# Kernel tuning notes

Measured on AMD Instinct MI355X. Metric: run time of the kernel, lower is better.

The kernel has to match this reference:

```python
import jax, jax.numpy as jnp
import numpy as np

# Sizes from init_kwargs / input_specs
D_MODEL = 1024; D_INT = 64; KW = 32; B = 2; L = 4096
SAMPLING = np.array([5, 5, 2, 1, 1]); DILATIONS = np.array([1, 1, 2, 4, 8])
SUBHEADS = len(SAMPLING); HEADS = int(SAMPLING.sum())  # 5, 14
HEAD_OF_SUB = np.repeat(np.arange(SUBHEADS), SAMPLING)  # subhead index for each head
HEAD_DIL = np.repeat(DILATIONS, SAMPLING)                # dilation for each head


def _win_idx(dil):
    # centered dilated band, clipped at sequence edges -> [L, KW]
    offs = (np.arange(KW) - KW // 2) * dil
    return np.clip(np.arange(L)[:, None] + offs[None, :], 0, L - 1)

SUB_IDX = jnp.asarray(np.stack([_win_idx(d) for d in DILATIONS]))  # [SUBHEADS, L, KW]
HEAD_IDX = jnp.asarray(np.stack([_win_idx(d) for d in HEAD_DIL]))  # [HEADS, L, KW]


def setup_inputs() -> dict:
    rng = jax.random.key(0)
    ks = jax.random.split(rng, 9)
    n = lambda i, sh, sc=1.0: jax.random.normal(ks[i], sh, dtype=jnp.float32) * sc
    return dict(
        query=n(0, (B, L, D_MODEL)),
        key=n(1, (B, L, D_MODEL)),
        value=n(2, (B, L, D_MODEL)),
        Wq=n(3, (SUBHEADS, D_MODEL, D_INT), 0.02),
        bq=jnp.zeros((SUBHEADS, D_INT), jnp.float32),
        Wk=n(4, (SUBHEADS, D_MODEL, D_INT), 0.02),
        bk=jnp.zeros((SUBHEADS, D_INT), jnp.float32),
        Wv=n(5, (HEADS, D_MODEL, D_INT), 0.02),
        bv=jnp.zeros((HEADS, D_INT), jnp.float32),
        Ws=n(6, (HEADS, KW, KW), 0.05) + jnp.eye(KW, dtype=jnp.float32)[None],
        bs=jnp.zeros((HEADS, KW), jnp.float32),
        Wc=n(7, (HEADS * D_INT, D_MODEL), 0.02),
        bc=jnp.zeros((D_MODEL,), jnp.float32),
    )


def reference(query, key, value, Wq, bq, Wk, bk, Wv, bv, Ws, bs, Wc, bc):
    # per-subhead query/key projections: [S, B, L, Di]
    q = jnp.einsum('bld,sdi->sbli', query, Wq) + bq[:, None, None, :]
    k = jnp.einsum('bld,sdi->sbli', key, Wk) + bk[:, None, None, :]
    # per-head value projection: [H, B, L, Di]
    v = jnp.einsum('bld,hdi->hbli', value, Wv) + bv[:, None, None, :]
    # dilated banded key windows per subhead: [S, B, L, KW, Di]
    kw = jax.vmap(lambda kh, ix: kh[:, ix], in_axes=(0, 0))(k, SUB_IDX)
    # banded scores [S, B, L, KW]
    scores = jnp.einsum('sbli,sblki->sblk', q, kw) / jnp.sqrt(jnp.float32(D_INT))
    # supersample: replicate each subhead's scores to its heads -> [H, B, L, KW]
    scores_h = scores[HEAD_OF_SUB]
    # per-head positional supersampling linear on the score window
    sampled = jnp.einsum('hblk,hkm->hblm', scores_h, Ws) + bs[:, None, None, :]
    attn = jax.nn.softmax(sampled, axis=-1)
    # dilated value windows per head: [H, B, L, KW, Di]
    vw = jax.vmap(lambda vh, ix: vh[:, ix], in_axes=(0, 0))(v, HEAD_IDX)
    out = jnp.einsum('hblk,hblki->hbli', attn, vw)  # [H, B, L, Di]
    out = jnp.transpose(out, (1, 2, 0, 3)).reshape(B, L, HEADS * D_INT)
    return out @ Wc + bc  # [B, L, D_MODEL]
```

## Files before the change

kernel.cpp:

```cpp
#include <hip/hip_runtime.h>
#include <math.h>

#define D_MODEL 1024
#define D_INT   64
#define KW      32
#define L_SEQ   4096
#define SUBHEADS 5
#define HEADS   14
#define M_ROWS  8192
#define N_CAT   896
#define NQK     320

typedef unsigned short us;
typedef unsigned int   uu;
typedef __attribute__((ext_vector_type(4))) unsigned int uu4;
typedef __attribute__((ext_vector_type(8))) short bf16x8_t;
typedef __attribute__((ext_vector_type(4))) float f32x4_t;

__device__ __forceinline__ float u2f(uu u) {
    float f; __builtin_memcpy(&f, &u, 4); return f;
}
__device__ __forceinline__ float blo(uu u) { return u2f(u << 16); }
__device__ __forceinline__ float bhi(uu u) { return u2f(u & 0xffff0000u); }
__device__ __forceinline__ us f2b(float f) {
    uu u; __builtin_memcpy(&u, &f, 4);
    u += 0x7fffu + ((u >> 16) & 1u);
    return (us)(u >> 16);
}
__device__ __forceinline__ uu pack2(float a, float b) {
    return (uu)f2b(a) | ((uu)f2b(b) << 16);
}
__device__ __forceinline__ uu cvtpk(float a, float b) {
    uu r;
    asm("v_cvt_pk_bf16_f32 %0, %1, %2" : "=v"(r) : "v"(a), "v"(b));
    return r;
}
__device__ __forceinline__ void load16(void* lds, const void* g) {
    __builtin_amdgcn_global_load_lds(
        (const __attribute__((address_space(1))) unsigned int*)g,
        (__attribute__((address_space(3))) unsigned int*)lds, 16, 0, 0);
}
__device__ __forceinline__ int subhead_of(int h) {
    return (h < 5) ? 0 : (h < 10) ? 1 : (h < 12) ? 2 : (h == 12) ? 3 : 4;
}
__device__ __forceinline__ int dil_of_sub(int s) {
    return (s <= 1) ? 1 : (1 << (s - 1));
}

#define CAST_BLK 1536
__global__ __launch_bounds__(256)
void prep_kernel(const float4* __restrict__ q, const float4* __restrict__ k,
                 const float4* __restrict__ v,
                 const float* __restrict__ Wq, const float* __restrict__ Wk,
                 const float* __restrict__ Wv, const float* __restrict__ Wc,
                 us* __restrict__ Xq, us* __restrict__ Xk, us* __restrict__ Xv,
                 us* __restrict__ Wqt, us* __restrict__ Wkt,
                 us* __restrict__ Wvt, us* __restrict__ Wct)
{
    __shared__ float t[32][33];
    const int tid = threadIdx.x;
    const int b = blockIdx.x;

    if (b < CAST_BLK) {
        const int arr = b >> 9;
        const int blk = b & 511;
        const float4* s = (arr == 0) ? q : (arr == 1) ? k : v;
        uu4* d = (uu4*)((arr == 0) ? Xq : (arr == 1) ? Xk : Xv);
        const int tg = blk * 256 + tid;
#pragma unroll
        for (int it = 0; it < 8; it++) {
            const int i = tg + it * 131072;
            float4 x0 = s[2 * i];
            float4 x1 = s[2 * i + 1];
            uu4 o;
            o.x = cvtpk(x0.x, x0.y); o.y = cvtpk(x0.z, x0.w);
            o.z = cvtpk(x1.x, x1.y); o.w = cvtpk(x1.z, x1.w);
            d[i] = o;
        }
        return;
    }

    int g = b - CAST_BLK;
    const float* S; us* D; int K, N;
    if (g < 640) {
        if (g < 320) { S = Wq; D = Wqt; } else { S = Wk; D = Wkt; g -= 320; }
        K = 1024; N = 64;
    } else if (g < 1536) {
        g -= 640; S = Wv; D = Wvt; K = 1024; N = 64;
    } else {
        g -= 1536; S = Wc; D = Wct; K = 896; N = 1024;
    }
    const int nkx = K >> 5;
    const int kx = g % nkx;
    const int rest = g / nkx;
    const int ny = rest % (N >> 5);
    const int z  = rest / (N >> 5);
    const int k0 = kx * 32, n0 = ny * 32;
    S += (size_t)z * K * N;
    D += (size_t)z * K * N;
    const int tx = tid & 31, ty = tid >> 5;
#pragma unroll
    for (int r = 0; r < 32; r += 8)
        t[r + ty][tx] = S[(size_t)(k0 + r + ty) * N + n0 + tx];
    __syncthreads();
#pragma unroll
    for (int r = 0; r < 32; r += 8)
        D[(size_t)(n0 + r + ty) * K + k0 + tx] = f2b(t[tx][r + ty]);
}

__device__ __forceinline__
void gemm64_core(const us* __restrict__ A, const us* __restrict__ Bt,
                 const float* __restrict__ bias, us* __restrict__ C,
                 int K, int ldC, int row0, int col0, us* As, us* Bs)
{
    const int tid = threadIdx.x, w = tid >> 6, lane = tid & 63;
    const int m = lane & 15, quad = lane >> 4;
    const int sr = lane >> 3;
    const int scs = (lane & 7) ^ sr;

    f32x4_t z4 = {0.f, 0.f, 0.f, 0.f};
    f32x4_t acc[2][4] = {{z4, z4, z4, z4}, {z4, z4, z4, z4}};

    for (int k0 = 0; k0 < K; k0 += 64) {
#pragma unroll
        for (int p = 0; p < 4; p++) {
            const int r = w * 32 + p * 8 + sr;
            load16(&As[(w * 32 + p * 8) * 64], A + (size_t)(row0 + r) * K + k0 + scs * 8);
        }
#pragma unroll
        for (int p = 0; p < 2; p++) {
            const int r = w * 16 + p * 8 + sr;
            load16(&Bs[(w * 16 + p * 8) * 64], Bt + (size_t)(col0 + r) * K + k0 + scs * 8);
        }
        __syncthreads();
#pragma unroll
        for (int ks = 0; ks < 2; ks++) {
            const int slot = ((ks * 4 + quad) ^ (m & 7)) * 8;
            bf16x8_t a0 = *(const bf16x8_t*)&As[(w * 32 + m) * 64 + slot];
            bf16x8_t a1 = *(const bf16x8_t*)&As[(w * 32 + 16 + m) * 64 + slot];
#pragma unroll
            for (int t = 0; t < 4; t++) {
                bf16x8_t bb = *(const bf16x8_t*)&Bs[(t * 16 + m) * 64 + slot];
                acc[0][t] = __builtin_amdgcn_mfma_f32_16x16x32_bf16(a0, bb, acc[0][t], 0, 0, 0);
                acc[1][t] = __builtin_amdgcn_mfma_f32_16x16x32_bf16(a1, bb, acc[1][t], 0, 0, 0);
            }
        }
        __syncthreads();
    }

#pragma unroll
    for (int tm = 0; tm < 2; tm++) {
        const int rbase = row0 + w * 32 + tm * 16 + quad * 4;
#pragma unroll
        for (int t = 0; t < 4; t++) {
            const int col = col0 + t * 16 + m;
            const float bi = bias[col];
#pragma unroll
            for (int r = 0; r < 4; r++)
                C[(size_t)(rbase + r) * ldC + col] = f2b(acc[tm][t][r] + bi);
        }
    }
}

__device__ __forceinline__
void gemm128_core(const us* __restrict__ A, const us* __restrict__ Bt,
                  const float* __restrict__ bias, void* __restrict__ Cv,
                  int K, int ldC, int outBf16, int row0, int col0,
                  us* As, us* Bs)
{
    const int tid = threadIdx.x, w = tid >> 6, lane = tid & 63;
    const int m = lane & 15, quad = lane >> 4;
    const int sr = lane >> 3;
    const int scs = (lane & 7) ^ sr;
    const int mrow0 = (w & 1) * 64, ncol0 = (w >> 1) * 64;

    f32x4_t z = {0.f, 0.f, 0.f, 0.f};
    f32x4_t acc[4][4] = {{z,z,z,z},{z,z,z,z},{z,z,z,z},{z,z,z,z}};

    for (int k0 = 0; k0 < K; k0 += 64) {
#pragma unroll
        for (int p = 0; p < 4; p++) {
            const int r = w * 32 + p * 8 + sr;
            load16(&As[(w * 32 + p * 8) * 64], A  + (size_t)(row0 + r) * K + k0 + scs * 8);
            load16(&Bs[(w * 32 + p * 8) * 64], Bt + (size_t)(col0 + r) * K + k0 + scs * 8);
        }
        __syncthreads();
#pragma unroll
        for (int ks = 0; ks < 2; ks++) {
            const int slot = ((ks * 4 + quad) ^ (m & 7)) * 8;
            bf16x8_t a[4], b[4];
#pragma unroll
            for (int t = 0; t < 4; t++) {
                a[t] = *(const bf16x8_t*)&As[(mrow0 + t * 16 + m) * 64 + slot];
                b[t] = *(const bf16x8_t*)&Bs[(ncol0 + t * 16 + m) * 64 + slot];
            }
#pragma unroll
            for (int i = 0; i < 4; i++)
#pragma unroll
                for (int j = 0; j < 4; j++)
                    acc[i][j] = __builtin_amdgcn_mfma_f32_16x16x32_bf16(a[i], b[j], acc[i][j], 0, 0, 0);
        }
        __syncthreads();
    }

#pragma unroll
    for (int i = 0; i < 4; i++) {
        const int rbase = row0 + mrow0 + i * 16 + quad * 4;
        if (outBf16) {
            us* Cb = (us*)Cv;
#pragma unroll
            for (int j = 0; j < 4; j++) {
                const int col = col0 + ncol0 + j * 16 + m;
                const float bi = bias[col];
#pragma unroll
                for (int r = 0; r < 4; r++)
                    Cb[(size_t)(rbase + r) * ldC + col] = f2b(acc[i][j][r] + bi);
            }
        } else {
            float* Cb = (float*)Cv;
#pragma unroll
            for (int j = 0; j < 4; j++) {
                const int col = col0 + ncol0 + j * 16 + m;
                const float bi = bias[col];
#pragma unroll
                for (int r = 0; r < 4; r++)
                    Cb[(size_t)(rbase + r) * ldC + col] = acc[i][j][r] + bi;
            }
        }
    }
}

__global__ __launch_bounds__(256)
void proj_kernel(const us* __restrict__ Xq, const us* __restrict__ Xk,
                 const us* __restrict__ Xv,
                 const us* __restrict__ Wqt, const us* __restrict__ Wkt,
                 const us* __restrict__ Wvt,
                 const float* __restrict__ bq, const float* __restrict__ bk,
                 const float* __restrict__ bv,
                 us* __restrict__ qbuf, us* __restrict__ kbuf,
                 us* __restrict__ vbuf)
{
    __shared__ us As[128 * 64];
    __shared__ us Bs[128 * 64];
    const int b = blockIdx.x;
    if (b < 448) {
        const int bx = b & 63, cy = b >> 6;
        gemm128_core(Xv, Wvt, bv, vbuf, D_MODEL, N_CAT, 1,
                     bx << 7, cy << 7, As, Bs);
    } else {
        const int idx = b - 448;
        const int bx = idx & 63;
        const int rest = idx >> 6;
        const int cy = rest % 5, z = rest / 5;
        gemm64_core(z ? Xk : Xq, z ? Wkt : Wqt, z ? bk : bq,
                    z ? kbuf : qbuf, D_MODEL, NQK,
                    bx << 7, cy << 6, As, Bs);
    }
}

__global__ __launch_bounds__(256)
void gemm_out(const us* __restrict__ ab, const us* __restrict__ Wct,
              const float* __restrict__ bc, float* __restrict__ out)
{
    __shared__ us As[128 * 64];
    __shared__ us Bs[128 * 64];
    gemm128_core(ab, Wct, bc, out, N_CAT, D_MODEL, 0,
                 (int)(blockIdx.x << 7), (int)(blockIdx.y << 7), As, Bs);
}

template<int ROWS>
__global__ __launch_bounds__(256)
void score_kernel(const us* __restrict__ qb, const us* __restrict__ kb,
                  float* __restrict__ scores, int sbase)
{
    __shared__ uu kslab[ROWS * 36];
    __shared__ uu qslab[64 * 32];

    const int tid  = threadIdx.x;
    const int wave = tid >> 6;
    const int lane = tid & 63;
    const int j    = lane & 31;
    const int half = lane >> 5;
    const int s    = sbase + blockIdx.y;
    const int d    = dil_of_sub(s);
    const int ml0  = blockIdx.x * 64;
    const int l0   = ml0 & 4095;
    const int bm   = ml0 - l0;
    const int W    = 64 + 31 * d;

    const uu* kg = (const uu*)kb;
    const uu* qg = (const uu*)qb;

    for (int idx = tid; idx < W * 32; idx += 256) {
        int r = idx >> 5, c = idx & 31;
        int src = l0 - 16 * d + r;
        src = src < 0 ? 0 : (src > 4095 ? 4095 : src);
        kslab[r * 36 + c] = kg[(size_t)(bm + src) * 160 + s * 32 + c];
    }
    for (int idx = tid; idx < 64 * 32; idx += 256) {
        int r = idx >> 5, c = idx & 31;
        qslab[r * 32 + c] = qg[(size_t)(ml0 + r) * 160 + s * 32 + c];
    }
    __syncthreads();

#pragma unroll
    for (int i = 0; i < 8; i++) {
        const int p = wave * 16 + i * 2 + half;
        const uu4* k4 = (const uu4*)&kslab[(p + j * d) * 36];
        const uu4* q4 = (const uu4*)&qslab[p * 32];
        float acc = 0.f;
#pragma unroll
        for (int q = 0; q < 8; q++) {
            uu4 kd = k4[q];
            uu4 qd = q4[q];
            acc = fmaf(blo(kd.x), blo(qd.x), acc); acc = fmaf(bhi(kd.x), bhi(qd.x), acc);
            acc = fmaf(blo(kd.y), blo(qd.y), acc); acc = fmaf(bhi(kd.y), bhi(qd.y), acc);
            acc = fmaf(blo(kd.z), blo(qd.z), acc); acc = fmaf(bhi(kd.z), bhi(qd.z), acc);
            acc = fmaf(blo(kd.w), blo(qd.w), acc); acc = fmaf(bhi(kd.w), bhi(qd.w), acc);
        }
        scores[((size_t)s * M_ROWS + ml0 + p) * 32 + j] = acc * 0.125f;
    }
}

template<int ROWS>
__global__ __launch_bounds__(256)
void head_kernel(const float* __restrict__ scores, const us* __restrict__ vb,
                 const float* __restrict__ Ws, const float* __restrict__ bs,
                 us* __restrict__ ab, int hbase)
{
    __shared__ uu    vslab[ROWS * 36];
    __shared__ float sab[64 * 36];

    const int tid  = threadIdx.x;
    const int wave = tid >> 6;
    const int lane = tid & 63;
    const int j    = lane & 31;
    const int half = lane >> 5;
    const int h    = hbase + blockIdx.y;
    const int s    = subhead_of(h);
    const int d    = dil_of_sub(s);
    const int ml0  = blockIdx.x * 64;
    const int l0   = ml0 & 4095;
    const int bm   = ml0 - l0;
    const int W    = 64 + 31 * d;

    const uu* vg = (const uu*)vb;
    for (int idx = tid; idx < W * 32; idx += 256) {
        int r = idx >> 5, c = idx & 31;
        int src = l0 - 16 * d + r;
        src = src < 0 ? 0 : (src > 4095 ? 4095 : src);
        vslab[r * 36 + c] = vg[(size_t)(bm + src) * 448 + h * 32 + c];
    }
    {
        const float4* g4 = (const float4*)(scores + ((size_t)s * M_ROWS + ml0) * 32);
#pragma unroll
        for (int t = 0; t < 2; t++) {
            int i4 = t * 256 + tid;
            int r = i4 >> 3, c4 = i4 & 7;
            *(float4*)&sab[r * 36 + c4 * 4] = g4[i4];
        }
    }
    float wsr[32];
#pragma unroll
    for (int k = 0; k < 32; k++) wsr[k] = Ws[(size_t)h * 1024 + k * 32 + j];
    const float bsv = bs[h * 32 + j];
    __syncthreads();

#pragma unroll
    for (int i = 0; i < 8; i++) {
        const int p = wave * 16 + i * 2 + half;
        const float4* s4 = (const float4*)&sab[p * 36];
        float acc = bsv;
#pragma unroll
        for (int q = 0; q < 8; q++) {
            float4 v = s4[q];
            acc = fmaf(v.x, wsr[q * 4 + 0], acc);
            acc = fmaf(v.y, wsr[q * 4 + 1], acc);
            acc = fmaf(v.z, wsr[q * 4 + 2], acc);
            acc = fmaf(v.w, wsr[q * 4 + 3], acc);
        }
        float mx = acc;
#pragma unroll
        for (int off = 16; off > 0; off >>= 1) mx = fmaxf(mx, __shfl_xor(mx, off, 64));
        float ex = __expf(acc - mx);
        float sum = ex;
#pragma unroll
        for (int off = 16; off > 0; off >>= 1) sum += __shfl_xor(sum, off, 64);
        sab[p * 36 + j] = ex / sum;
    }

    const int o = lane >> 3;
    const int c = lane & 7;
#pragma unroll
    for (int pass = 0; pass < 2; pass++) {
        const int p  = wave * 16 + pass * 8 + o;
        const int ml = ml0 + p;
        float a0 = 0.f, a1 = 0.f, a2 = 0.f, a3 = 0.f;
        float a4 = 0.f, a5 = 0.f, a6 = 0.f, a7 = 0.f;
#pragma unroll
        for (int mm = 0; mm < 32; mm++) {
            const float at = sab[p * 36 + mm];
            uu4 vd = *(const uu4*)&vslab[(p + mm * d) * 36 + c * 4];
            a0 = fmaf(blo(vd.x), at, a0); a1 = fmaf(bhi(vd.x), at, a1);
            a2 = fmaf(blo(vd.y), at, a2); a3 = fmaf(bhi(vd.y), at, a3);
            a4 = fmaf(blo(vd.z), at, a4); a5 = fmaf(bhi(vd.z), at, a5);
            a6 = fmaf(blo(vd.w), at, a6); a7 = fmaf(bhi(vd.w), at, a7);
        }
        uu4 od;
        od.x = pack2(a0, a1); od.y = pack2(a2, a3);
        od.z = pack2(a4, a5); od.w = pack2(a6, a7);
        *(uu4*)&((uu*)ab)[(size_t)ml * 448 + h * 32 + c * 4] = od;
    }
}

extern "C" void kernel_launch(void* const* d_in, const int* in_sizes, int n_in,
                              void* d_out, int out_size, void* d_ws, size_t ws_size,
                              hipStream_t stream)
{
    const float* query = (const float*)d_in[0];
    const float* key   = (const float*)d_in[1];
    const float* value = (const float*)d_in[2];
    const float* Wq    = (const float*)d_in[3];
    const float* bq    = (const float*)d_in[4];
    const float* Wk    = (const float*)d_in[5];
    const float* bk    = (const float*)d_in[6];
    const float* Wv    = (const float*)d_in[7];
    const float* bv    = (const float*)d_in[8];
    const float* Ws    = (const float*)d_in[9];
    const float* bs    = (const float*)d_in[10];
    const float* Wc    = (const float*)d_in[11];
    const float* bc    = (const float*)d_in[12];
    float* out = (float*)d_out;

    us* w = (us*)d_ws;
    us* Xq  = w;
    us* ab  = w;
    us* Xk  = Xq  + (size_t)M_ROWS * D_MODEL;
    float* scores = (float*)Xk;
    us* Xv  = Xk  + (size_t)M_ROWS * D_MODEL;
    us* Wqt = Xv  + (size_t)M_ROWS * D_MODEL;
    us* Wkt = Wqt + (size_t)SUBHEADS * D_INT * D_MODEL;
    us* Wvt = Wkt + (size_t)SUBHEADS * D_INT * D_MODEL;
    us* Wct = Wvt + (size_t)HEADS * D_INT * D_MODEL;
    us* qbuf = Wct + (size_t)D_MODEL * N_CAT;
    us* kbuf = qbuf + (size_t)M_ROWS * NQK;
    us* vbuf = kbuf + (size_t)M_ROWS * NQK;

    dim3 blk(256);

    prep_kernel<<<dim3(CAST_BLK + 2432), blk, 0, stream>>>(
        (const float4*)query, (const float4*)key, (const float4*)value,
        Wq, Wk, Wv, Wc, Xq, Xk, Xv, Wqt, Wkt, Wvt, Wct);

    proj_kernel<<<dim3(1088), blk, 0, stream>>>(
        Xq, Xk, Xv, Wqt, Wkt, Wvt, bq, bk, bv, qbuf, kbuf, vbuf);

    score_kernel<126><<<dim3(M_ROWS / 64, 3), blk, 0, stream>>>(qbuf, kbuf, scores, 0);
    score_kernel<312><<<dim3(M_ROWS / 64, 2), blk, 0, stream>>>(qbuf, kbuf, scores, 3);

    head_kernel<312><<<dim3(M_ROWS / 64, 2),  blk, 0, stream>>>(scores, vbuf, Ws, bs, ab, 12);
    head_kernel<126><<<dim3(M_ROWS / 64, 12), blk, 0, stream>>>(scores, vbuf, Ws, bs, ab, 0);

    gemm_out<<<dim3(M_ROWS / 128, D_MODEL / 128), blk, 0, stream>>>(
        ab, Wct, bc, out);
}
```

Before: 290.1 us.

## Fuse score and head kernels into per-subhead attention kernel

Merges the score and head kernels into one attn_kernel per subhead. Each block keeps its scores in LDS and loops over that subhead's heads, reusing the scores for each head's supersampling, softmax and value aggregation. This removes the fp32 score round-trip through global memory and two launches, and the slab loads now use 16-byte vectors. In exchange the grid shrinks sharply: subheads 0 and 1 get only 256 blocks, each running 5 heads serially with no overlap of loads and compute, which can leave CUs idle and unbalance the work.

```diff
diff --git a/kernel.cpp b/kernel.cpp
--- a/kernel.cpp
+++ b/kernel.cpp
@@ -40,11 +40,14 @@
         (const __attribute__((address_space(1))) unsigned int*)g,
         (__attribute__((address_space(3))) unsigned int*)lds, 16, 0, 0);
 }
-__device__ __forceinline__ int subhead_of(int h) {
-    return (h < 5) ? 0 : (h < 10) ? 1 : (h < 12) ? 2 : (h == 12) ? 3 : 4;
-}
 __device__ __forceinline__ int dil_of_sub(int s) {
     return (s <= 1) ? 1 : (1 << (s - 1));
+}
+__device__ __forceinline__ int hstart_of_sub(int s) {
+    return (s == 0) ? 0 : (s == 1) ? 5 : (s == 2) ? 10 : (s == 3) ? 12 : 13;
+}
+__device__ __forceinline__ int hcount_of_sub(int s) {
+    return (s <= 1) ? 5 : (s == 2) ? 2 : 1;
 }
 
 #define CAST_BLK 1536
@@ -270,11 +273,18 @@
 
 template<int ROWS>
 __global__ __launch_bounds__(256)
-void score_kernel(const us* __restrict__ qb, const us* __restrict__ kb,
-                  float* __restrict__ scores, int sbase)
-{
-    __shared__ uu kslab[ROWS * 36];
-    __shared__ uu qslab[64 * 32];
+void attn_kernel(const us* __restrict__ qb, const us* __restrict__ kb,
+                 const us* __restrict__ vb,
+                 const float* __restrict__ Ws, const float* __restrict__ bs,
+                 us* __restrict__ ab, int sbase)
+{
+    __shared__ uu    kq[ROWS * 36 + 64 * 32];
+    __shared__ float sab[64 * 36];
+    __shared__ float atn[64 * 36];
+
+    uu* kslab = kq;
+    uu* qslab = kq + ROWS * 36;
+    uu* vslab = kq;
 
     const int tid  = threadIdx.x;
     const int wave = tid >> 6;
@@ -288,18 +298,17 @@
     const int bm   = ml0 - l0;
     const int W    = 64 + 31 * d;
 
-    const uu* kg = (const uu*)kb;
-    const uu* qg = (const uu*)qb;
-
-    for (int idx = tid; idx < W * 32; idx += 256) {
-        int r = idx >> 5, c = idx & 31;
+    const uu4* kg4 = (const uu4*)kb;
+    const uu4* qg4 = (const uu4*)qb;
+    for (int idx = tid; idx < W * 8; idx += 256) {
+        int r = idx >> 3, c4 = idx & 7;
         int src = l0 - 16 * d + r;
         src = src < 0 ? 0 : (src > 4095 ? 4095 : src);
-        kslab[r * 36 + c] = kg[(size_t)(bm + src) * 160 + s * 32 + c];
-    }
-    for (int idx = tid; idx < 64 * 32; idx += 256) {
-        int r = idx >> 5, c = idx & 31;
-        qslab[r * 32 + c] = qg[(size_t)(ml0 + r) * 160 + s * 32 + c];
+        *(uu4*)&kslab[r * 36 + c4 * 4] = kg4[(size_t)(bm + src) * 40 + s * 8 + c4];
+    }
+    for (int idx = tid; idx < 64 * 8; idx += 256) {
+        int r = idx >> 3, c4 = idx & 7;
+        *(uu4*)&qslab[r * 32 + c4 * 4] = qg4[(size_t)(ml0 + r) * 40 + s * 8 + c4];
     }
     __syncthreads();
 
@@ -318,98 +327,73 @@
             acc = fmaf(blo(kd.z), blo(qd.z), acc); acc = fmaf(bhi(kd.z), bhi(qd.z), acc);
             acc = fmaf(blo(kd.w), blo(qd.w), acc); acc = fmaf(bhi(kd.w), bhi(qd.w), acc);
         }
-        scores[((size_t)s * M_ROWS + ml0 + p) * 32 + j] = acc * 0.125f;
-    }
-}
-
-template<int ROWS>
-__global__ __launch_bounds__(256)
-void head_kernel(const float* __restrict__ scores, const us* __restrict__ vb,
-                 const float* __restrict__ Ws, const float* __restrict__ bs,
-                 us* __restrict__ ab, int hbase)
-{
-    __shared__ uu    vslab[ROWS * 36];
-    __shared__ float sab[64 * 36];
-
-    const int tid  = threadIdx.x;
-    const int wave = tid >> 6;
-    const int lane = tid & 63;
-    const int j    = lane & 31;
-    const int half = lane >> 5;
-    const int h    = hbase + blockIdx.y;
-    const int s    = subhead_of(h);
-    const int d    = dil_of_sub(s);
-    const int ml0  = blockIdx.x * 64;
-    const int l0   = ml0 & 4095;
-    const int bm   = ml0 - l0;
-    const int W    = 64 + 31 * d;
-
-    const uu* vg = (const uu*)vb;
-    for (int idx = tid; idx < W * 32; idx += 256) {
-        int r = idx >> 5, c = idx & 31;
-        int src = l0 - 16 * d + r;
-        src = src < 0 ? 0 : (src > 4095 ? 4095 : src);
-        vslab[r * 36 + c] = vg[(size_t)(bm + src) * 448 + h * 32 + c];
-    }
-    {
-        const float4* g4 = (const float4*)(scores + ((size_t)s * M_ROWS + ml0) * 32);
-#pragma unroll
-        for (int t = 0; t < 2; t++) {
-            int i4 = t * 256 + tid;
-            int r = i4 >> 3, c4 = i4 & 7;
-            *(float4*)&sab[r * 36 + c4 * 4] = g4[i4];
-        }
-    }
-    float wsr[32];
-#pragma unroll
-    for (int k = 0; k < 32; k++) wsr[k] = Ws[(size_t)h * 1024 + k * 32 + j];
-    const float bsv = bs[h * 32 + j];
+        sab[p * 36 + j] = acc * 0.125f;
+    }
     __syncthreads();
 
-#pragma unroll
-    for (int i = 0; i < 8; i++) {
-        const int p = wave * 16 + i * 2 + half;
-        const float4* s4 = (const float4*)&sab[p * 36];
-        float acc = bsv;
-#pragma unroll
-        for (int q = 0; q < 8; q++) {
-            float4 v = s4[q];
-            acc = fmaf(v.x, wsr[q * 4 + 0], acc);
-            acc = fmaf(v.y, wsr[q * 4 + 1], acc);
-            acc = fmaf(v.z, wsr[q * 4 + 2], acc);
-            acc = fmaf(v.w, wsr[q * 4 + 3], acc);
-        }
-        float mx = acc;
-#pragma unroll
-        for (int off = 16; off > 0; off >>= 1) mx = fmaxf(mx, __shfl_xor(mx, off, 64));
-        float ex = __expf(acc - mx);
-        float sum = ex;
-#pragma unroll
-        for (int off = 16; off > 0; off >>= 1) sum += __shfl_xor(sum, off, 64);
-        sab[p * 36 + j] = ex / sum;
-    }
-
-    const int o = lane >> 3;
-    const int c = lane & 7;
-#pragma unroll
-    for (int pass = 0; pass < 2; pass++) {
-        const int p  = wave * 16 + pass * 8 + o;
-        const int ml = ml0 + p;
-        float a0 = 0.f, a1 = 0.f, a2 = 0.f, a3 = 0.f;
-        float a4 = 0.f, a5 = 0.f, a6 = 0.f, a7 = 0.f;
-#pragma unroll
-        for (int mm = 0; mm < 32; mm++) {
-            const float at = sab[p * 36 + mm];
-            uu4 vd = *(const uu4*)&vslab[(p + mm * d) * 36 + c * 4];
-            a0 = fmaf(blo(vd.x), at, a0); a1 = fmaf(bhi(vd.x), at, a1);
-            a2 = fmaf(blo(vd.y), at, a2); a3 = fmaf(bhi(vd.y), at, a3);
-            a4 = fmaf(blo(vd.z), at, a4); a5 = fmaf(bhi(vd.z), at, a5);
-            a6 = fmaf(blo(vd.w), at, a6); a7 = fmaf(bhi(vd.w), at, a7);
-        }
-        uu4 od;
-        od.x = pack2(a0, a1); od.y = pack2(a2, a3);
-        od.z = pack2(a4, a5); od.w = pack2(a6, a7);
-        *(uu4*)&((uu*)ab)[(size_t)ml * 448 + h * 32 + c * 4] = od;
+    const int h0 = hstart_of_sub(s);
+    const int hc = hcount_of_sub(s);
+    const uu4* vg4 = (const uu4*)vb;
+
+    for (int hh = h0; hh < h0 + hc; hh++) {
+        for (int idx = tid; idx < W * 8; idx += 256) {
+            int r = idx >> 3, c4 = idx & 7;
+            int src = l0 - 16 * d + r;
+            src = src < 0 ? 0 : (src > 4095 ? 4095 : src);
+            *(uu4*)&vslab[r * 36 + c4 * 4] = vg4[(size_t)(bm + src) * 112 + hh * 8 + c4];
+        }
+        float wsr[32];
+#pragma unroll
+        for (int k = 0; k < 32; k++) wsr[k] = Ws[(size_t)hh * 1024 + k * 32 + j];
+        const float bsv = bs[hh * 32 + j];
+
+#pragma unroll
+        for (int i = 0; i < 8; i++) {
+            const int p = wave * 16 + i * 2 + half;
+            const float4* s4 = (const float4*)&sab[p * 36];
+            float acc = bsv;
+#pragma unroll
+            for (int q = 0; q < 8; q++) {
+                float4 v = s4[q];
+                acc = fmaf(v.x, wsr[q * 4 + 0], acc);
+                acc = fmaf(v.y, wsr[q * 4 + 1], acc);
+                acc = fmaf(v.z, wsr[q * 4 + 2], acc);
+                acc = fmaf(v.w, wsr[q * 4 + 3], acc);
+            }
+            float mx = acc;
+#pragma unroll
+            for (int off = 16; off > 0; off >>= 1) mx = fmaxf(mx, __shfl_xor(mx, off, 64));
+            float ex = __expf(acc - mx);
+            float sum = ex;
+#pragma unroll
+            for (int off = 16; off > 0; off >>= 1) sum += __shfl_xor(sum, off, 64);
+            atn[p * 36 + j] = ex / sum;
+        }
+        __syncthreads();
+
+        const int o = lane >> 3;
+        const int c = lane & 7;
+#pragma unroll
+        for (int pass = 0; pass < 2; pass++) {
+            const int p  = wave * 16 + pass * 8 + o;
+            const int ml = ml0 + p;
+            float a0 = 0.f, a1 = 0.f, a2 = 0.f, a3 = 0.f;
+            float a4 = 0.f, a5 = 0.f, a6 = 0.f, a7 = 0.f;
+#pragma unroll
+            for (int mm = 0; mm < 32; mm++) {
+                const float at = atn[p * 36 + mm];
+                uu4 vd = *(const uu4*)&vslab[(p + mm * d) * 36 + c * 4];
+                a0 = fmaf(blo(vd.x), at, a0); a1 = fmaf(bhi(vd.x), at, a1);
+                a2 = fmaf(blo(vd.y), at, a2); a3 = fmaf(bhi(vd.y), at, a3);
+                a4 = fmaf(blo(vd.z), at, a4); a5 = fmaf(bhi(vd.z), at, a5);
+                a6 = fmaf(blo(vd.w), at, a6); a7 = fmaf(bhi(vd.w), at, a7);
+            }
+            uu4 od;
+            od.x = pack2(a0, a1); od.y = pack2(a2, a3);
+            od.z = pack2(a4, a5); od.w = pack2(a6, a7);
+            *(uu4*)&((uu*)ab)[(size_t)ml * 448 + hh * 32 + c * 4] = od;
+        }
+        __syncthreads();
     }
 }
 
@@ -436,7 +420,6 @@
     us* Xq  = w;
     us* ab  = w;
     us* Xk  = Xq  + (size_t)M_ROWS * D_MODEL;
-    float* scores = (float*)Xk;
     us* Xv  = Xk  + (size_t)M_ROWS * D_MODEL;
     us* Wqt = Xv  + (size_t)M_ROWS * D_MODEL;
     us* Wkt = Wqt + (size_t)SUBHEADS * D_INT * D_MODEL;
@@ -455,11 +438,10 @@
     proj_kernel<<<dim3(1088), blk, 0, stream>>>(
         Xq, Xk, Xv, Wqt, Wkt, Wvt, bq, bk, bv, qbuf, kbuf, vbuf);
 
-    score_kernel<126><<<dim3(M_ROWS / 64, 3), blk, 0, stream>>>(qbuf, kbuf, scores, 0);
-    score_kernel<312><<<dim3(M_ROWS / 64, 2), blk, 0, stream>>>(qbuf, kbuf, scores, 3);
-
-    head_kernel<312><<<dim3(M_ROWS / 64, 2),  blk, 0, stream>>>(scores, vbuf, Ws, bs, ab, 12);
-    head_kernel<126><<<dim3(M_ROWS / 64, 12), blk, 0, stream>>>(scores, vbuf, Ws, bs, ab, 0);
+    attn_kernel<95><<<dim3(M_ROWS / 64, 2), blk, 0, stream>>>(
+        qbuf, kbuf, vbuf, Ws, bs, ab, 0);
+    attn_kernel<312><<<dim3(M_ROWS / 64, 3), blk, 0, stream>>>(
+        qbuf, kbuf, vbuf, Ws, bs, ab, 2);
 
     gemm_out<<<dim3(M_ROWS / 128, D_MODEL / 128), blk, 0, stream>>>(
         ab, Wct, bc, out);
```

Measured after the change: 304.3 us. 1.05x slower.
